# Kernel tuning notes

Hardware: AMD Instinct MI355X
Metric: run time of the kernel (lower is better)

## Reference

```python
import jax, jax.numpy as jnp
import numpy as np

N_GAUSS = 16  # matches init_kwargs n_gaussians


def _so3_forward(z, n):
    # z: [B, 6n]. First 3n entries -> axis params, rest -> logvar logits.
    v = z[:, :3 * n].reshape(-1, n, 3)
    a, b, c = v[..., 0], v[..., 1], v[..., 2]
    zero = jnp.zeros_like(a)
    # antisym_matrix: A = [[0, a, b], [-a, 0, c], [-b, -c, 0]]  (skew-symmetric)
    A = jnp.stack([
        jnp.stack([zero, a, b], axis=-1),
        jnp.stack([-a, zero, c], axis=-1),
        jnp.stack([-b, -c, zero], axis=-1),
    ], axis=-2)  # [B, n, 3, 3]
    # matrix_exp of a skew-symmetric 3x3 == Rodrigues formula (exact):
    # exp(A) = I + sin(t)/t * A + (1-cos(t))/t^2 * A^2, t = ||(a,b,c)||
    th2 = a * a + b * b + c * c
    small = th2 < 1e-8
    t2 = jnp.where(small, jnp.ones_like(th2), th2)  # safe denom
    t = jnp.sqrt(t2)
    s1 = jnp.where(small, 1.0 - th2 / 6.0, jnp.sin(t) / t)
    s2 = jnp.where(small, 0.5 - th2 / 24.0, (1.0 - jnp.cos(t)) / t2)
    A2 = A @ A  # [B, n, 3, 3]
    I = jnp.eye(3, dtype=z.dtype)
    mean = I + s1[..., None, None] * A + s2[..., None, None] * A2
    logvar = 5.4 * jax.nn.sigmoid(z[:, 3 * n:].reshape(-1, n, 3)) - 9.2
    return mean, logvar


def setup_inputs() -> dict:
    key = jax.random.key(0)
    B = 262144
    z = jax.random.normal(key, (B, 6 * N_GAUSS), dtype=jnp.float32)
    return {"z": z}


def reference(z):
    return _so3_forward(z, N_GAUSS)
```

## Files before the change

kernel.cpp:

```cpp
#include <hip/hip_runtime.h>


#define BLOCK 256

typedef float f4 __attribute__((ext_vector_type(4)));

__global__ __launch_bounds__(BLOCK) void so3_encode_kernel(
    const float* __restrict__ z,
    float* __restrict__ out_mean,
    float* __restrict__ out_logvar)
{
    __shared__ float lds_m[BLOCK * 36];
    __shared__ float lds_l[BLOCK * 12];

    const int t    = threadIdx.x;
    const int lane = t & 63;
    const int wave = t >> 6;
    const int idx  = blockIdx.x * BLOCK + t;
    const int b    = idx >> 2;
    const int k    = idx & 3;

    const f4* za = reinterpret_cast<const f4*>(z + (size_t)b * 96 + k * 12);
    f4 a0 = za[0];
    f4 a1 = za[1];
    f4 a2 = za[2];
    const f4* zl = reinterpret_cast<const f4*>(z + (size_t)b * 96 + 48 + k * 12);
    f4 l0 = zl[0];
    f4 l1 = zl[1];
    f4 l2 = zl[2];

    float av[12] = {a0.x, a0.y, a0.z, a0.w,
                    a1.x, a1.y, a1.z, a1.w,
                    a2.x, a2.y, a2.z, a2.w};
    float lv[12] = {l0.x, l0.y, l0.z, l0.w,
                    l1.x, l1.y, l1.z, l1.w,
                    l2.x, l2.y, l2.z, l2.w};

    float m[36];
    #pragma unroll
    for (int j = 0; j < 4; ++j) {
        float a  = av[3 * j + 0];
        float bb = av[3 * j + 1];
        float c  = av[3 * j + 2];
        float th2 = a * a + bb * bb + c * c;
        bool small = th2 < 1e-8f;
        float t2 = small ? 1.0f : th2;
        float tt = sqrtf(t2);
        float sn, cs;
        __sincosf(tt, &sn, &cs);
        float inv_t2 = 1.0f / t2;
        float s1 = small ? (1.0f - th2 * (1.0f / 6.0f))  : (sn * tt * inv_t2);
        float s2 = small ? (0.5f - th2 * (1.0f / 24.0f)) : ((1.0f - cs) * inv_t2);

        float* o = m + 9 * j;
        float ab = a * bb, ac = a * c, bc = bb * c;
        o[0] = 1.0f - s2 * (a * a + bb * bb);
        o[1] = s1 * a  - s2 * bc;
        o[2] = s1 * bb + s2 * ac;
        o[3] = -s1 * a - s2 * bc;
        o[4] = 1.0f - s2 * (a * a + c * c);
        o[5] = s1 * c  - s2 * ab;
        o[6] = -s1 * bb + s2 * ac;
        o[7] = -s1 * c  - s2 * ab;
        o[8] = 1.0f - s2 * (bb * bb + c * c);
    }

    float lg[12];
    #pragma unroll
    for (int j = 0; j < 12; ++j) {
        lg[j] = 5.4f / (1.0f + __expf(-lv[j])) - 9.2f;
    }

    f4* lm = reinterpret_cast<f4*>(lds_m + wave * (64 * 36) + lane * 36);
    #pragma unroll
    for (int q = 0; q < 9; ++q) {
        f4 v = {m[4 * q + 0], m[4 * q + 1], m[4 * q + 2], m[4 * q + 3]};
        lm[q] = v;
    }

    f4* ll = reinterpret_cast<f4*>(lds_l + wave * (64 * 12) + lane * 12);
    #pragma unroll
    for (int q = 0; q < 3; ++q) {
        f4 v = {lg[4 * q + 0], lg[4 * q + 1], lg[4 * q + 2], lg[4 * q + 3]};
        ll[q] = v;
    }

    asm volatile("s_waitcnt lgkmcnt(0)" ::: "memory");
    __builtin_amdgcn_sched_barrier(0);

    const f4* lmw = reinterpret_cast<const f4*>(lds_m + wave * (64 * 36));
    f4* om = reinterpret_cast<f4*>(out_mean)
           + (size_t)blockIdx.x * (BLOCK * 9) + wave * (64 * 9);
    #pragma unroll
    for (int i = 0; i < 9; ++i)
        om[i * 64 + lane] = lmw[i * 64 + lane];

    const f4* llw = reinterpret_cast<const f4*>(lds_l + wave * (64 * 12));
    f4* ol = reinterpret_cast<f4*>(out_logvar)
           + (size_t)blockIdx.x * (BLOCK * 3) + wave * (64 * 3);
    #pragma unroll
    for (int i = 0; i < 3; ++i)
        ol[i * 64 + lane] = llw[i * 64 + lane];
}

extern "C" void kernel_launch(void* const* d_in, const int* in_sizes, int n_in,
                              void* d_out, int out_size, void* d_ws, size_t ws_size,
                              hipStream_t stream) {
    const float* z = (const float*)d_in[0];
    const int B = in_sizes[0] / 96;
    float* out_mean = (float*)d_out;
    float* out_logvar = (float*)d_out + (size_t)B * 16 * 9;

    const int nthreads = B * 4;
    const int grid = nthreads / BLOCK;
    so3_encode_kernel<<<grid, BLOCK, 0, stream>>>(z, out_mean, out_logvar);
}
```

Before: 54.02 us.

## Map one thread per Gaussian instead of four per thread

Each thread now handles a single Gaussian (16 threads per batch row) rather than four, loading six scalars instead of vectorised f4 loads. LDS use per block drops sharply and a min-blocks launch bound of 8 is added to raise occupancy. The LDS-staged coalesced store is kept, using partial-lane f4 writes. The trade-off is more threads, scalar strided global loads, and 4x more blocks to launch.

```diff
diff --git a/kernel.cpp b/kernel.cpp
--- a/kernel.cpp
+++ b/kernel.cpp
@@ -5,102 +5,70 @@
 
 typedef float f4 __attribute__((ext_vector_type(4)));
 
-__global__ __launch_bounds__(BLOCK) void so3_encode_kernel(
+__global__ __launch_bounds__(BLOCK, 8) void so3_encode_kernel(
     const float* __restrict__ z,
     float* __restrict__ out_mean,
     float* __restrict__ out_logvar)
 {
-    __shared__ float lds_m[BLOCK * 36];
-    __shared__ float lds_l[BLOCK * 12];
+    __shared__ float smean[4][64 * 9];
+    __shared__ float slv[4][64 * 3];
 
     const int t    = threadIdx.x;
     const int lane = t & 63;
-    const int wave = t >> 6;
-    const int idx  = blockIdx.x * BLOCK + t;
-    const int b    = idx >> 2;
-    const int k    = idx & 3;
+    const int w    = t >> 6;
+    const int g    = blockIdx.x * BLOCK + t;
+    const int b    = g >> 4;
+    const int s    = g & 15;
 
-    const f4* za = reinterpret_cast<const f4*>(z + (size_t)b * 96 + k * 12);
-    f4 a0 = za[0];
-    f4 a1 = za[1];
-    f4 a2 = za[2];
-    const f4* zl = reinterpret_cast<const f4*>(z + (size_t)b * 96 + 48 + k * 12);
-    f4 l0 = zl[0];
-    f4 l1 = zl[1];
-    f4 l2 = zl[2];
+    const float* zr = z + (size_t)b * 96 + s * 3;
+    float a  = zr[0];
+    float bb = zr[1];
+    float c  = zr[2];
+    float x0 = zr[48];
+    float x1 = zr[49];
+    float x2 = zr[50];
 
-    float av[12] = {a0.x, a0.y, a0.z, a0.w,
-                    a1.x, a1.y, a1.z, a1.w,
-                    a2.x, a2.y, a2.z, a2.w};
-    float lv[12] = {l0.x, l0.y, l0.z, l0.w,
-                    l1.x, l1.y, l1.z, l1.w,
-                    l2.x, l2.y, l2.z, l2.w};
+    float th2 = a * a + bb * bb + c * c;
+    bool small = th2 < 1e-8f;
+    float t2 = small ? 1.0f : th2;
+    float tt = sqrtf(t2);
+    float sn, cs;
+    __sincosf(tt, &sn, &cs);
+    float inv_t2 = 1.0f / t2;
+    float s1 = small ? (1.0f - th2 * (1.0f / 6.0f))  : (sn * tt * inv_t2);
+    float s2 = small ? (0.5f - th2 * (1.0f / 24.0f)) : ((1.0f - cs) * inv_t2);
 
-    float m[36];
-    #pragma unroll
-    for (int j = 0; j < 4; ++j) {
-        float a  = av[3 * j + 0];
-        float bb = av[3 * j + 1];
-        float c  = av[3 * j + 2];
-        float th2 = a * a + bb * bb + c * c;
-        bool small = th2 < 1e-8f;
-        float t2 = small ? 1.0f : th2;
-        float tt = sqrtf(t2);
-        float sn, cs;
-        __sincosf(tt, &sn, &cs);
-        float inv_t2 = 1.0f / t2;
-        float s1 = small ? (1.0f - th2 * (1.0f / 6.0f))  : (sn * tt * inv_t2);
-        float s2 = small ? (0.5f - th2 * (1.0f / 24.0f)) : ((1.0f - cs) * inv_t2);
+    float ab = a * bb, ac = a * c, bc = bb * c;
+    float* sm = &smean[w][lane * 9];
+    sm[0] = 1.0f - s2 * (a * a + bb * bb);
+    sm[1] = s1 * a  - s2 * bc;
+    sm[2] = s1 * bb + s2 * ac;
+    sm[3] = -s1 * a - s2 * bc;
+    sm[4] = 1.0f - s2 * (a * a + c * c);
+    sm[5] = s1 * c  - s2 * ab;
+    sm[6] = -s1 * bb + s2 * ac;
+    sm[7] = -s1 * c  - s2 * ab;
+    sm[8] = 1.0f - s2 * (bb * bb + c * c);
 
-        float* o = m + 9 * j;
-        float ab = a * bb, ac = a * c, bc = bb * c;
-        o[0] = 1.0f - s2 * (a * a + bb * bb);
-        o[1] = s1 * a  - s2 * bc;
-        o[2] = s1 * bb + s2 * ac;
-        o[3] = -s1 * a - s2 * bc;
-        o[4] = 1.0f - s2 * (a * a + c * c);
-        o[5] = s1 * c  - s2 * ab;
-        o[6] = -s1 * bb + s2 * ac;
-        o[7] = -s1 * c  - s2 * ab;
-        o[8] = 1.0f - s2 * (bb * bb + c * c);
-    }
-
-    float lg[12];
-    #pragma unroll
-    for (int j = 0; j < 12; ++j) {
-        lg[j] = 5.4f / (1.0f + __expf(-lv[j])) - 9.2f;
-    }
-
-    f4* lm = reinterpret_cast<f4*>(lds_m + wave * (64 * 36) + lane * 36);
-    #pragma unroll
-    for (int q = 0; q < 9; ++q) {
-        f4 v = {m[4 * q + 0], m[4 * q + 1], m[4 * q + 2], m[4 * q + 3]};
-        lm[q] = v;
-    }
-
-    f4* ll = reinterpret_cast<f4*>(lds_l + wave * (64 * 12) + lane * 12);
-    #pragma unroll
-    for (int q = 0; q < 3; ++q) {
-        f4 v = {lg[4 * q + 0], lg[4 * q + 1], lg[4 * q + 2], lg[4 * q + 3]};
-        ll[q] = v;
-    }
+    float* sl = &slv[w][lane * 3];
+    sl[0] = 5.4f / (1.0f + __expf(-x0)) - 9.2f;
+    sl[1] = 5.4f / (1.0f + __expf(-x1)) - 9.2f;
+    sl[2] = 5.4f / (1.0f + __expf(-x2)) - 9.2f;
 
     asm volatile("s_waitcnt lgkmcnt(0)" ::: "memory");
     __builtin_amdgcn_sched_barrier(0);
 
-    const f4* lmw = reinterpret_cast<const f4*>(lds_m + wave * (64 * 36));
-    f4* om = reinterpret_cast<f4*>(out_mean)
-           + (size_t)blockIdx.x * (BLOCK * 9) + wave * (64 * 9);
-    #pragma unroll
-    for (int i = 0; i < 9; ++i)
-        om[i * 64 + lane] = lmw[i * 64 + lane];
+    const int g_base = blockIdx.x * BLOCK + (w << 6);
 
-    const f4* llw = reinterpret_cast<const f4*>(lds_l + wave * (64 * 12));
-    f4* ol = reinterpret_cast<f4*>(out_logvar)
-           + (size_t)blockIdx.x * (BLOCK * 3) + wave * (64 * 3);
-    #pragma unroll
-    for (int i = 0; i < 3; ++i)
-        ol[i * 64 + lane] = llw[i * 64 + lane];
+    const f4* smv = reinterpret_cast<const f4*>(&smean[w][0]);
+    f4* om = reinterpret_cast<f4*>(out_mean + (size_t)g_base * 9);
+    om[lane]      = smv[lane];
+    om[64 + lane] = smv[64 + lane];
+    if (lane < 16) om[128 + lane] = smv[128 + lane];
+
+    const f4* slvv = reinterpret_cast<const f4*>(&slv[w][0]);
+    f4* ol = reinterpret_cast<f4*>(out_logvar + (size_t)g_base * 3);
+    if (lane < 48) ol[lane] = slvv[lane];
 }
 
 extern "C" void kernel_launch(void* const* d_in, const int* in_sizes, int n_in,
@@ -111,7 +79,7 @@
     float* out_mean = (float*)d_out;
     float* out_logvar = (float*)d_out + (size_t)B * 16 * 9;
 
-    const int nthreads = B * 4;
+    const int nthreads = B * 16;
     const int grid = nthreads / BLOCK;
     so3_encode_kernel<<<grid, BLOCK, 0, stream>>>(z, out_mean, out_logvar);
 }
```

Measured after the change: 51.62 us, median of 2. 4.4% less time.
